# Optimization experiments

Measured on AMD Instinct MI355X. Metric: run time of the kernel, lower is better.

## Reference

```python
import jax, jax.numpy as jnp
import numpy as np

N = 100_000   # nodes (batched over G graphs)
E = 3_200_000 # edges (avg degree 32)
G = 64        # graphs in the batch
IN_FEATS, H1, H3, NUM_CLASSES = 64, 64, 64, 2


def setup_inputs() -> dict:
    key = jax.random.key(0)
    ks = jax.random.split(key, 11)
    return {
        "in_feat": jax.random.normal(ks[0], (N, IN_FEATS), jnp.float32),
        "edge_weights": jax.random.uniform(ks[1], (E,), jnp.float32, 1e-3, 1.0),
        "W1": jax.random.normal(ks[2], (IN_FEATS, H1), jnp.float32) / np.sqrt(IN_FEATS),
        "b1": jnp.zeros((H1,), jnp.float32),
        "W2": jax.random.normal(ks[3], (H1, H3), jnp.float32) / np.sqrt(H1),
        "b2": jnp.zeros((H3,), jnp.float32),
        "Wc": jax.random.normal(ks[4], (H3, NUM_CLASSES), jnp.float32) / np.sqrt(H3),
        "bc": jnp.zeros((NUM_CLASSES,), jnp.float32),
        "edge_src": jax.random.randint(ks[5], (E,), 0, N, jnp.int32),
        "edge_dst": jax.random.randint(ks[6], (E,), 0, N, jnp.int32),
        "graph_ids": jnp.sort(jax.random.randint(ks[7], (N,), 0, G, jnp.int32)),
    }


def reference(in_feat, edge_weights, W1, b1, W2, b2, Wc, bc,
              edge_src, edge_dst, graph_ids):
    # EdgeWeightNorm(norm='right'): w_e / (sum of weights into dst(e))
    deg_w = jax.ops.segment_sum(edge_weights, edge_dst, num_segments=N)  # [N]
    nw = edge_weights / deg_w[edge_dst]                                  # [E]

    # unweighted in-degree used by SAGEConv 'gcn' aggregator
    deg = jax.ops.segment_sum(jnp.ones((E,), jnp.float32), edge_dst, num_segments=N)  # [N]

    def sage_gcn(h, W, b):
        # weighted neighbor sum: sum_e nw_e * h[src_e] scattered to dst
        msg = h[edge_src] * nw[:, None]                                  # [E, F]
        neigh = jax.ops.segment_sum(msg, edge_dst, num_segments=N)      # [N, F]
        h_neigh = (neigh + h) / (deg[:, None] + 1.0)                     # gcn: include self, /(deg+1)
        return h_neigh @ W + b                                           # fc_neigh + bias

    h = jax.nn.relu(sage_gcn(in_feat, W1, b1))
    h = jax.nn.relu(sage_gcn(h, W2, b2))

    # dgl.mean_nodes: per-graph mean of node features
    counts = jax.ops.segment_sum(jnp.ones((N,), jnp.float32), graph_ids, num_segments=G)
    hg = jax.ops.segment_sum(h, graph_ids, num_segments=G) / jnp.maximum(counts, 1.0)[:, None]

    return hg @ Wc + bc  # [G, num_classes]
```

## Files before the change

### kernel.cpp

```cpp
#include <hip/hip_runtime.h>
#include <hip/hip_fp16.h>


#define CH2  4096
#define BK   1024
#define NB   128
#define CAPB 5120
#define CAPP 6144
#define SRCMASK ((1 << 18) - 1)
#define SRC17   0x1FFFFu

__device__ __forceinline__ float readlane_f(float v, int l) {
    return __int_as_float(__builtin_amdgcn_readlane(__float_as_int(v), l));
}

__device__ __forceinline__ int2 ntload_i2(const int2* p) {
    unsigned long long r = __builtin_nontemporal_load((const unsigned long long*)p);
    return make_int2((int)(unsigned)(r & 0xffffffffull), (int)(unsigned)(r >> 32));
}

__device__ __forceinline__ void ntstore_f2(float2* p, float2 v) {
    union { float2 f; unsigned long long u; } c;
    c.f = v;
    __builtin_nontemporal_store(c.u, (unsigned long long*)p);
}

__global__ void k_cvt(const float4* __restrict__ x, uint2* __restrict__ xh, int n4) {
    int i = blockIdx.x * blockDim.x + threadIdx.x;
    if (i >= n4) return;
    float4 v = x[i];
    __half2 a = __floats2half2_rn(v.x, v.y);
    __half2 b = __floats2half2_rn(v.z, v.w);
    uint2 r;
    r.x = *(const unsigned*)&a;
    r.y = *(const unsigned*)&b;
    xh[i] = r;
}

__global__ __launch_bounds__(512) void k_binfill2(
        const int* __restrict__ esrc, const int* __restrict__ edst,
        const float* __restrict__ ew, int* __restrict__ cursor,
        int2* __restrict__ bsw, int E, int B) {
    __shared__ int2 stg[CH2];
    __shared__ int h[BK];
    __shared__ int lcur[BK];
    __shared__ int gb[BK];
    __shared__ int sc[512];
    const int tid = threadIdx.x;

    for (int i = tid; i < BK; i += 512) h[i] = 0;
    __syncthreads();
    int e0 = blockIdx.x * CH2;
    int e1 = min(E, e0 + CH2);
    for (int e = e0 + tid; e < e1; e += 512)
        atomicAdd(&h[edst[e] >> 7], 1);
    __syncthreads();
    int a0 = h[2 * tid], a1 = h[2 * tid + 1];
    int s  = a0 + a1;
    sc[tid] = s;
    __syncthreads();
    for (int off = 1; off < 512; off <<= 1) {
        int t = (tid >= off) ? sc[tid - off] : 0;
        __syncthreads();
        sc[tid] += t;
        __syncthreads();
    }
    int base = sc[tid] - s;
    lcur[2 * tid]     = base;
    lcur[2 * tid + 1] = base + a0;
    gb[2 * tid]     = a0 ? atomicAdd(&cursor[2 * tid],     a0) : 0;
    gb[2 * tid + 1] = a1 ? atomicAdd(&cursor[2 * tid + 1], a1) : 0;
    __syncthreads();
    for (int e = e0 + tid; e < e1; e += 512) {
        int d = edst[e];
        int b = d >> 7;
        int p = atomicAdd(&lcur[b], 1);
        stg[p] = make_int2(((d & 127) << 18) | esrc[e], __float_as_int(ew[e]));
    }
    __syncthreads();
    const int wid = tid >> 6, lane = tid & 63;
    for (int b = wid; b < B; b += 8) {
        int len = h[b];
        if (!len) continue;
        int lb = lcur[b] - len;
        int g  = gb[b];
        int wlen = min(len, CAPB - g);
        if (wlen <= 0) continue;
        size_t gbase = (size_t)b * CAPB + g;
        for (int i = lane; i < wlen; i += 64)
            bsw[gbase + i] = stg[lb + i];
    }
}

__global__ __launch_bounds__(512) void k_csrsort(
        const int2* __restrict__ bsw, const int* __restrict__ cursor,
        unsigned* __restrict__ csr, int* __restrict__ off, int* __restrict__ fill,
        int N) {
    __shared__ unsigned se[CAPP];
    __shared__ int cur[NB];
    __shared__ int pfx[NB];
    __shared__ int tot;
    const int b = blockIdx.x, tid = threadIdx.x;
    for (int i = tid; i < CAPP; i += 512) se[i] = 0u;
    if (tid < NB) cur[tid] = 0;
    __syncthreads();
    const int cnt = min(cursor[b], CAPB);
    const int2* __restrict__ eb = bsw + (size_t)b * CAPB;
    for (int i = tid; i < cnt; i += 512)
        atomicAdd(&cur[eb[i].x >> 18], 1);
    __syncthreads();
    int pc = 0;
    if (tid < NB) {
        int c0 = cur[tid & ~1], c1 = cur[tid | 1];
        pc = (max(c0, c1) + 7) & ~7;
        pfx[tid] = pc;
    }
    __syncthreads();
    for (int o = 1; o < NB; o <<= 1) {
        int t = 0;
        if (tid < NB && tid >= o) t = pfx[tid - o];
        __syncthreads();
        if (tid < NB) pfx[tid] += t;
        __syncthreads();
    }
    if (tid < NB) {
        int excl = pfx[tid] - pc;
        int node = b * NB + tid;
        if (node < N) { off[node] = b * CAPP + excl; fill[node] = cur[tid]; }
        cur[tid] = excl;
        if (tid == NB - 1) tot = min(pfx[tid], CAPP);
    }
    __syncthreads();
    for (int i = tid; i < cnt; i += 512) {
        int2 e = eb[i];
        int p = atomicAdd(&cur[e.x >> 18], 1);
        unsigned h15 = (unsigned)__half_as_ushort(
                           __float2half_rn(__int_as_float(e.y))) & 0x7FFFu;
        if (p < CAPP)
            se[p] = ((unsigned)e.x & SRC17) | (h15 << 17);
    }
    __syncthreads();
    const int T = tot;
    unsigned* __restrict__ cb = csr + (size_t)b * CAPP;
    for (int i = tid; i < T; i += 512) cb[i] = se[i];
}

__global__ void k_fill_pad(const int* __restrict__ esrc, const int* __restrict__ edst,
                           const float* __restrict__ ew, int* __restrict__ fill,
                           int2* __restrict__ csr, int E, int CAP) {
    int e = blockIdx.x * blockDim.x + threadIdx.x;
    if (e < E) {
        int d = edst[e];
        int p = atomicAdd(&fill[d], 1);
        if (p < CAP)
            csr[(size_t)d * CAP + p] = make_int2(esrc[e], __float_as_int(ew[e]));
    }
}

__global__ void k_cnt(const int* __restrict__ edst, int* __restrict__ cnt, int E) {
    int e = blockIdx.x * blockDim.x + threadIdx.x;
    if (e < E) atomicAdd(&cnt[edst[e]], 1);
}

__global__ void k_off(const int* __restrict__ cnt, int* __restrict__ off,
                      int* __restrict__ fill, int* __restrict__ cursor, int N) {
    int i    = blockIdx.x * blockDim.x + threadIdx.x;
    int lane = threadIdx.x & 63;
    int c    = (i < N) ? cnt[i] : 0;
    int pref = c;
    #pragma unroll
    for (int d = 1; d < 64; d <<= 1) {
        int t = __shfl_up(pref, d);
        if (lane >= d) pref += t;
    }
    int total = __shfl(pref, 63);
    int base  = 0;
    if (lane == 63) base = atomicAdd(cursor, total);
    base = __shfl(base, 63);
    if (i < N) {
        int p = base + pref - c;
        off[i]  = p;
        fill[i] = p;
    }
}

__global__ void k_fill(const int* __restrict__ esrc, const int* __restrict__ edst,
                       const float* __restrict__ ew, int* __restrict__ fill,
                       int2* __restrict__ csr, int E) {
    int e = blockIdx.x * blockDim.x + threadIdx.x;
    if (e < E) {
        int d = edst[e];
        int p = atomicAdd(&fill[d], 1);
        csr[p] = make_int2(esrc[e], __float_as_int(ew[e]));
    }
}

__global__ __launch_bounds__(256, 6) void k_agg_p(
        const unsigned* __restrict__ xh, const int* __restrict__ off,
        const int* __restrict__ cnt_arr, const unsigned* __restrict__ csr,
        float* __restrict__ agg, int N) {
    const int lane = threadIdx.x & 63;
    const int slot = lane >> 5;
    const int f8   = lane & 31;
    const int wq   = (blockIdx.x * blockDim.x + threadIdx.x) >> 6;
    const int nw   = (gridDim.x * blockDim.x) >> 6;
    const int npair = (N + 1) >> 1;

    for (int pr = wq; pr < npair; pr += nw) {
        const int  node  = 2 * pr + slot;
        const bool valid = node < N;
        const int  cnt_s = valid ? cnt_arr[node] : 0;
        const int  st_s  = valid ? off[node] : 0;
        const int  cA = __builtin_amdgcn_readlane(cnt_s, 0);
        const int  cB = __builtin_amdgcn_readlane(cnt_s, 32);
        const int  pc = (max(cA, cB) + 7) & ~7;

        float2 acc = {0.f, 0.f};
        float  sw  = 0.f;
        const unsigned* __restrict__ pS = csr + st_s;
        for (int k = 0; k < pc; k += 8) {
            uint4 e0 = *(const uint4*)(pS + k);
            uint4 e1 = *(const uint4*)(pS + k + 4);
            unsigned ev[8] = {e0.x, e0.y, e0.z, e0.w, e1.x, e1.y, e1.z, e1.w};
            float    w[8];
            unsigned u[8];
            #pragma unroll
            for (int t = 0; t < 8; ++t) {
                unsigned e = ev[t];
                w[t] = __half2float(__ushort_as_half((unsigned short)(e >> 17)));
                u[t] = xh[((e & SRC17) << 5) | (unsigned)f8];
            }
            #pragma unroll
            for (int t = 0; t < 8; ++t) {
                float2 v = __half22float2(*(const __half2*)&u[t]);
                acc.x = fmaf(w[t], v.x, acc.x);
                acc.y = fmaf(w[t], v.y, acc.y);
                sw += w[t];
            }
        }
        if (valid) {
            float invw = (sw > 0.f) ? (1.f / sw) : 0.f;
            float invd = 1.f / ((float)cnt_s + 1.f);
            unsigned us = xh[((unsigned)node << 5) | (unsigned)f8];
            float2 xs = __half22float2(*(const __half2*)&us);
            float2 hn;
            hn.x = (acc.x * invw + xs.x) * invd;
            hn.y = (acc.y * invw + xs.y) * invd;
            ntstore_f2(&((float2*)agg)[(size_t)node * 32 + f8], hn);
        }
    }
}

__global__ __launch_bounds__(256, 4) void k_agg_f(
        const unsigned* __restrict__ xh, const int* __restrict__ off,
        const int* __restrict__ cnt_arr, const int2* __restrict__ csr,
        float* __restrict__ agg, int N, int CAP) {
    const int lane   = threadIdx.x & 63;
    const int slot   = lane >> 5;
    const int f8     = lane & 31;
    const int wave   = (blockIdx.x * blockDim.x + threadIdx.x) >> 6;
    const int nwaves = (gridDim.x * blockDim.x) >> 6;

    int node  = wave;
    int cnt_p = 0, start_p = 0;
    if (node < N) {
        cnt_p   = cnt_arr[node];
        start_p = (CAP > 0) ? node * CAP : off[node];
        if (CAP > 0) cnt_p = min(cnt_p, CAP);
    }
    for (; node < N; node += nwaves) {
        const int cnt = cnt_p, start = start_p;
        int nn = node + nwaves;
        if (nn < N) {
            cnt_p   = cnt_arr[nn];
            start_p = (CAP > 0) ? nn * CAP : off[nn];
            if (CAP > 0) cnt_p = min(cnt_p, CAP);
        }
        int2 ee = make_int2(0, 0);
        if (lane < cnt) ee = ntload_i2(&csr[start + lane]);
        float2 acc0 = {0.f, 0.f}, acc1 = {0.f, 0.f};
        float  sw = 0.0f;
        for (int bk = 0; bk < cnt; bk += 64) {
            int   s_l = ee.x;
            float w_l = __int_as_float(ee.y);
            int2 en = make_int2(0, 0);
            int  rem = cnt - bk - 64;
            if (lane < rem) en = ntload_i2(&csr[start + bk + 64 + lane]);
            sw += w_l;
            #pragma unroll
            for (int half = 0; half < 2; ++half) {
                float    w[16];
                unsigned u[16];
                #pragma unroll
                for (int k = 0; k < 16; ++k) {
                    int idx = half * 32 + 2 * k + slot;
                    int s   = __shfl(s_l, idx);
                    w[k]    = __shfl(w_l, idx);
                    u[k]    = xh[(size_t)s * 32 + f8];
                }
                #pragma unroll
                for (int k = 0; k < 16; k += 2) {
                    float2 v0 = __half22float2(*(const __half2*)&u[k]);
                    float2 v1 = __half22float2(*(const __half2*)&u[k + 1]);
                    acc0.x = fmaf(w[k],     v0.x, acc0.x);
                    acc0.y = fmaf(w[k],     v0.y, acc0.y);
                    acc1.x = fmaf(w[k + 1], v1.x, acc1.x);
                    acc1.y = fmaf(w[k + 1], v1.y, acc1.y);
                }
            }
            ee = en;
        }
        acc0.x += acc1.x; acc0.y += acc1.y;
        acc0.x += __shfl_xor(acc0.x, 32);
        acc0.y += __shfl_xor(acc0.y, 32);
        #pragma unroll
        for (int mask = 1; mask <= 32; mask <<= 1) sw += __shfl_xor(sw, mask);
        float invw = (sw > 0.0f) ? (1.0f / sw) : 0.0f;
        float invd = 1.0f / ((float)cnt + 1.0f);
        if (lane < 32) {
            unsigned us = xh[(size_t)node * 32 + f8];
            float2 xs = __half22float2(*(const __half2*)&us);
            float2 hn;
            hn.x = (acc0.x * invw + xs.x) * invd;
            hn.y = (acc0.y * invw + xs.y) * invd;
            ntstore_f2(&((float2*)agg)[(size_t)node * 32 + f8], hn);
        }
    }
}

__global__ __launch_bounds__(256) void k_fc(
        const float* __restrict__ agg, const float* __restrict__ W,
        const float* __restrict__ b, __half* __restrict__ outh, int N) {
    const int lane   = threadIdx.x & 63;
    const int wave   = (blockIdx.x * blockDim.x + threadIdx.x) >> 6;
    const int nwaves = (gridDim.x * blockDim.x) >> 6;
    float wc[64];
    #pragma unroll
    for (int f = 0; f < 64; ++f) wc[f] = W[f * 64 + lane];
    const float bias = b[lane];
    for (int node = wave; node < N; node += nwaves) {
        float hn = agg[(size_t)node * 64 + lane];
        float o0 = bias, o1 = 0.f, o2 = 0.f, o3 = 0.f;
        #pragma unroll
        for (int f = 0; f < 64; f += 4) {
            o0 = fmaf(readlane_f(hn, f),     wc[f],     o0);
            o1 = fmaf(readlane_f(hn, f + 1), wc[f + 1], o1);
            o2 = fmaf(readlane_f(hn, f + 2), wc[f + 2], o2);
            o3 = fmaf(readlane_f(hn, f + 3), wc[f + 3], o3);
        }
        float o = fmaxf((o0 + o1) + (o2 + o3), 0.0f);
        outh[(size_t)node * 64 + lane] = __float2half_rn(o);
    }
}

__global__ __launch_bounds__(256) void k_fcpool(
        const float* __restrict__ agg, const float* __restrict__ W,
        const float* __restrict__ b, const int* __restrict__ gid,
        float* __restrict__ hg, float* __restrict__ cntg, int N) {
    const int lane   = threadIdx.x & 63;
    const int wave   = (blockIdx.x * blockDim.x + threadIdx.x) >> 6;
    const int nwaves = (gridDim.x * blockDim.x) >> 6;
    float wc[64];
    #pragma unroll
    for (int f = 0; f < 64; ++f) wc[f] = W[f * 64 + lane];
    const float bias = b[lane];
    const int per   = (N + nwaves - 1) / nwaves;
    const int start = wave * per;
    const int end   = min(N, start + per);
    if (start >= N) return;

    int   curg = -1;
    float acc  = 0.0f;
    int   c    = 0;
    for (int node = start; node < end; ++node) {
        float hn = agg[(size_t)node * 64 + lane];
        float o0 = bias, o1 = 0.f, o2 = 0.f, o3 = 0.f;
        #pragma unroll
        for (int f = 0; f < 64; f += 4) {
            o0 = fmaf(readlane_f(hn, f),     wc[f],     o0);
            o1 = fmaf(readlane_f(hn, f + 1), wc[f + 1], o1);
            o2 = fmaf(readlane_f(hn, f + 2), wc[f + 2], o2);
            o3 = fmaf(readlane_f(hn, f + 3), wc[f + 3], o3);
        }
        float o = fmaxf((o0 + o1) + (o2 + o3), 0.0f);
        int g = gid[node];
        if (g != curg) {
            if (c > 0) {
                atomicAdd(&hg[curg * 64 + lane], acc);
                if (lane == 0) atomicAdd(&cntg[curg], (float)c);
            }
            curg = g; acc = 0.0f; c = 0;
        }
        acc += o;
        ++c;
    }
    if (c > 0) {
        atomicAdd(&hg[curg * 64 + lane], acc);
        if (lane == 0) atomicAdd(&cntg[curg], (float)c);
    }
}

__global__ void k_out(const float* __restrict__ hg, const float* __restrict__ cntg,
                      const float* __restrict__ Wc, const float* __restrict__ bc,
                      float* __restrict__ out, int G) {
    int t = blockIdx.x * blockDim.x + threadIdx.x;
    if (t >= G * 2) return;
    int g = t >> 1, c = t & 1;
    float ct = fmaxf(cntg[g], 1.0f);
    float o  = bc[c];
    for (int f = 0; f < 64; ++f)
        o += (hg[g * 64 + f] / ct) * Wc[f * 2 + c];
    out[t] = o;
}

extern "C" void kernel_launch(void* const* d_in, const int* in_sizes, int n_in,
                              void* d_out, int out_size, void* d_ws, size_t ws_size,
                              hipStream_t stream) {
    const float* in_feat = (const float*)d_in[0];
    const float* ew      = (const float*)d_in[1];
    const float* W1      = (const float*)d_in[2];
    const float* b1      = (const float*)d_in[3];
    const float* W2      = (const float*)d_in[4];
    const float* b2      = (const float*)d_in[5];
    const float* Wc      = (const float*)d_in[6];
    const float* bc      = (const float*)d_in[7];
    const int*   esrc    = (const int*)d_in[8];
    const int*   edst    = (const int*)d_in[9];
    const int*   gid     = (const int*)d_in[10];

    const int E = in_sizes[1];
    const int N = in_sizes[10];
    const int G = out_size / 2;
    float* outp = (float*)d_out;

    auto alignup = [](size_t x) { return (x + 15) & ~(size_t)15; };
    char* base = (char*)d_ws;
    const int FC_BLK = 1024, AGG_BLK = 2048;
    const int n4 = N * 16;

    const int B     = (N + NB - 1) / NB;
    const int NBLK2 = (E + CH2 - 1) / CH2;

    size_t zhdr  = ((size_t)G * 64 + G + BK) * 4;
    size_t o_off = alignup(zhdr);
    size_t o_fil = o_off + alignup((size_t)N * 4);
    size_t o_bsw = o_fil + alignup((size_t)N * 4);
    size_t o_csr = o_bsw + alignup((size_t)B * CAPB * 8);
    size_t o_t1  = o_csr + alignup((size_t)B * CAPP * 4);
    size_t o_t2  = o_t1 + alignup((size_t)N * 64 * 4);
    size_t o_xh  = o_t2 + alignup((size_t)N * 64 * 4);
    size_t o_th  = o_xh + alignup((size_t)N * 64 * 2);
    size_t needB = o_th + (size_t)N * 64 * 2;

    bool cap_ok = ((size_t)E / B) + 512 < CAPB && N <= (1 << 17);

    if (ws_size >= needB && B <= BK && cap_ok) {
        float*    hg     = (float*)base;
        float*    cntg   = hg + (size_t)G * 64;
        int*      cursor = (int*)(cntg + G);
        int*      off    = (int*)(base + o_off);
        int*      fill   = (int*)(base + o_fil);
        int2*     bsw    = (int2*)(base + o_bsw);
        unsigned* csr    = (unsigned*)(base + o_csr);
        float*    t1     = (float*)(base + o_t1);
        float*    t2     = (float*)(base + o_t2);
        unsigned* xh0    = (unsigned*)(base + o_xh);
        __half*   th1    = (__half*)(base + o_th);

        hipMemsetAsync(d_ws, 0, zhdr, stream);
        k_cvt     <<<(n4 + 255) / 256, 256, 0, stream>>>((const float4*)in_feat, (uint2*)xh0, n4);
        k_binfill2<<<NBLK2, 512, 0, stream>>>(esrc, edst, ew, cursor, bsw, E, B);
        k_csrsort <<<B, 512, 0, stream>>>(bsw, cursor, csr, off, fill, N);
        k_agg_p <<<AGG_BLK, 256, 0, stream>>>(xh0, off, fill, csr, t1, N);
        k_fc    <<<FC_BLK, 256, 0, stream>>>(t1, W1, b1, th1, N);
        k_agg_p <<<AGG_BLK, 256, 0, stream>>>((const unsigned*)th1, off, fill, csr, t2, N);
        k_fcpool<<<FC_BLK, 256, 0, stream>>>(t2, W2, b2, gid, hg, cntg, N);
        k_out   <<<1, 128, 0, stream>>>(hg, cntg, Wc, bc, outp, G);
        return;
    }

    const int CAP = 96;
    size_t hdr    = ((size_t)G * 64 + G + 1 + N) * 4;
    size_t needB2 = alignup(hdr) + alignup((size_t)N * CAP * 8)
                  + alignup((size_t)N * 64 * 4) * 2
                  + alignup((size_t)N * 64 * 2) * 2;
    if (ws_size >= needB2) {
        size_t o = 0;
        float* hg     = (float*)(base + o);
        float* cntg   = hg + (size_t)G * 64;
        int*   fill   = (int*)(cntg + G) + 1;
        o += alignup(hdr);
        int2*     csr = (int2*)(base + o);    o += alignup((size_t)N * CAP * 8);
        float*    t1  = (float*)(base + o);   o += alignup((size_t)N * 64 * 4);
        float*    t2  = (float*)(base + o);   o += alignup((size_t)N * 64 * 4);
        unsigned* xh0 = (unsigned*)(base + o); o += alignup((size_t)N * 64 * 2);
        __half*   th1 = (__half*)(base + o);

        hipMemsetAsync(d_ws, 0, hdr, stream);
        k_cvt     <<<(n4 + 255) / 256, 256, 0, stream>>>((const float4*)in_feat, (uint2*)xh0, n4);
        k_fill_pad<<<(E + 255) / 256, 256, 0, stream>>>(esrc, edst, ew, fill, csr, E, CAP);
        k_agg_f <<<AGG_BLK, 256, 0, stream>>>(xh0, (const int*)nullptr, fill, csr, t1, N, CAP);
        k_fc    <<<FC_BLK, 256, 0, stream>>>(t1, W1, b1, th1, N);
        k_agg_f <<<AGG_BLK, 256, 0, stream>>>((const unsigned*)th1, (const int*)nullptr, fill, csr, t2, N, CAP);
        k_fcpool<<<FC_BLK, 256, 0, stream>>>(t2, W2, b2, gid, hg, cntg, N);
        k_out   <<<1, 128, 0, stream>>>(hg, cntg, Wc, bc, outp, G);
        return;
    }

    {
        size_t o = 0;
        float* hg     = (float*)(base + o);
        float* cntg   = hg + (size_t)G * 64;
        int*   cursor = (int*)(cntg + G);
        int*   cnt    = cursor + 1;
        o += alignup(hdr);
        int*      off  = (int*)(base + o);    o += alignup((size_t)N * 4);
        int*      fill = (int*)(base + o);    o += alignup((size_t)N * 4);
        int2*     csr  = (int2*)(base + o);   o += alignup((size_t)E * 8);
        float*    t1   = (float*)(base + o);  o += alignup((size_t)N * 64 * 4);
        float*    t2   = (float*)(base + o);  o += alignup((size_t)N * 64 * 4);
        unsigned* xh0  = (unsigned*)(base + o); o += alignup((size_t)N * 64 * 2);
        __half*   th1  = (__half*)(base + o);

        hipMemsetAsync(d_ws, 0, hdr, stream);
        k_cvt <<<(n4 + 255) / 256, 256, 0, stream>>>((const float4*)in_feat, (uint2*)xh0, n4);
        k_cnt <<<(E + 255) / 256, 256, 0, stream>>>(edst, cnt, E);
        k_off <<<(N + 255) / 256, 256, 0, stream>>>(cnt, off, fill, cursor, N);
        k_fill<<<(E + 255) / 256, 256, 0, stream>>>(esrc, edst, ew, fill, csr, E);
        k_agg_f <<<AGG_BLK, 256, 0, stream>>>(xh0, off, cnt, csr, t1, N, 0);
        k_fc    <<<FC_BLK, 256, 0, stream>>>(t1, W1, b1, th1, N);
        k_agg_f <<<AGG_BLK, 256, 0, stream>>>((const unsigned*)th1, off, cnt, csr, t2, N, 0);
        k_fcpool<<<FC_BLK, 256, 0, stream>>>(t2, W2, b2, gid, hg, cntg, N);
        k_out   <<<1, 128, 0, stream>>>(hg, cntg, Wc, bc, outp, G);
    }
}
```

Measured before the change: 402.3 us.

## Replace two-pass bucketed CSR sort with count/scan/atomic-scatter CSR build

```diff
diff --git a/kernel.cpp b/kernel.cpp
--- a/kernel.cpp
+++ b/kernel.cpp
@@ -2,13 +2,7 @@
 #include <hip/hip_fp16.h>
 
 
-#define CH2  4096
-#define BK   1024
-#define NB   128
-#define CAPB 5120
-#define CAPP 6144
-#define SRCMASK ((1 << 18) - 1)
-#define SRC17   0x1FFFFu
+#define SRC17 0x1FFFFu
 
 __device__ __forceinline__ float readlane_f(float v, int l) {
     return __int_as_float(__builtin_amdgcn_readlane(__float_as_int(v), l));
@@ -37,112 +31,50 @@
     xh[i] = r;
 }
 
-__global__ __launch_bounds__(512) void k_binfill2(
-        const int* __restrict__ esrc, const int* __restrict__ edst,
-        const float* __restrict__ ew, int* __restrict__ cursor,
-        int2* __restrict__ bsw, int E, int B) {
-    __shared__ int2 stg[CH2];
-    __shared__ int h[BK];
-    __shared__ int lcur[BK];
-    __shared__ int gb[BK];
-    __shared__ int sc[512];
-    const int tid = threadIdx.x;
-
-    for (int i = tid; i < BK; i += 512) h[i] = 0;
-    __syncthreads();
-    int e0 = blockIdx.x * CH2;
-    int e1 = min(E, e0 + CH2);
-    for (int e = e0 + tid; e < e1; e += 512)
-        atomicAdd(&h[edst[e] >> 7], 1);
-    __syncthreads();
-    int a0 = h[2 * tid], a1 = h[2 * tid + 1];
-    int s  = a0 + a1;
-    sc[tid] = s;
-    __syncthreads();
-    for (int off = 1; off < 512; off <<= 1) {
-        int t = (tid >= off) ? sc[tid - off] : 0;
-        __syncthreads();
-        sc[tid] += t;
-        __syncthreads();
-    }
-    int base = sc[tid] - s;
-    lcur[2 * tid]     = base;
-    lcur[2 * tid + 1] = base + a0;
-    gb[2 * tid]     = a0 ? atomicAdd(&cursor[2 * tid],     a0) : 0;
-    gb[2 * tid + 1] = a1 ? atomicAdd(&cursor[2 * tid + 1], a1) : 0;
-    __syncthreads();
-    for (int e = e0 + tid; e < e1; e += 512) {
-        int d = edst[e];
-        int b = d >> 7;
-        int p = atomicAdd(&lcur[b], 1);
-        stg[p] = make_int2(((d & 127) << 18) | esrc[e], __float_as_int(ew[e]));
-    }
-    __syncthreads();
-    const int wid = tid >> 6, lane = tid & 63;
-    for (int b = wid; b < B; b += 8) {
-        int len = h[b];
-        if (!len) continue;
-        int lb = lcur[b] - len;
-        int g  = gb[b];
-        int wlen = min(len, CAPB - g);
-        if (wlen <= 0) continue;
-        size_t gbase = (size_t)b * CAPB + g;
-        for (int i = lane; i < wlen; i += 64)
-            bsw[gbase + i] = stg[lb + i];
-    }
-}
-
-__global__ __launch_bounds__(512) void k_csrsort(
-        const int2* __restrict__ bsw, const int* __restrict__ cursor,
-        unsigned* __restrict__ csr, int* __restrict__ off, int* __restrict__ fill,
-        int N) {
-    __shared__ unsigned se[CAPP];
-    __shared__ int cur[NB];
-    __shared__ int pfx[NB];
-    __shared__ int tot;
-    const int b = blockIdx.x, tid = threadIdx.x;
-    for (int i = tid; i < CAPP; i += 512) se[i] = 0u;
-    if (tid < NB) cur[tid] = 0;
-    __syncthreads();
-    const int cnt = min(cursor[b], CAPB);
-    const int2* __restrict__ eb = bsw + (size_t)b * CAPB;
-    for (int i = tid; i < cnt; i += 512)
-        atomicAdd(&cur[eb[i].x >> 18], 1);
-    __syncthreads();
-    int pc = 0;
-    if (tid < NB) {
-        int c0 = cur[tid & ~1], c1 = cur[tid | 1];
+__global__ void k_cnt(const int* __restrict__ edst, int* __restrict__ cnt, int E) {
+    int e = blockIdx.x * blockDim.x + threadIdx.x;
+    if (e < E) atomicAdd(&cnt[edst[e]], 1);
+}
+
+__global__ __launch_bounds__(256) void k_offp(
+        const int* __restrict__ cnt, int* __restrict__ off,
+        int* __restrict__ cursor, int N) {
+    const int i     = blockIdx.x * blockDim.x + threadIdx.x;
+    const int npair = (N + 1) >> 1;
+    const int lane  = threadIdx.x & 63;
+    int sz = 0, pc = 0;
+    if (i < npair) {
+        int c0 = cnt[2 * i];
+        int c1 = (2 * i + 1 < N) ? cnt[2 * i + 1] : 0;
         pc = (max(c0, c1) + 7) & ~7;
-        pfx[tid] = pc;
-    }
-    __syncthreads();
-    for (int o = 1; o < NB; o <<= 1) {
-        int t = 0;
-        if (tid < NB && tid >= o) t = pfx[tid - o];
-        __syncthreads();
-        if (tid < NB) pfx[tid] += t;
-        __syncthreads();
-    }
-    if (tid < NB) {
-        int excl = pfx[tid] - pc;
-        int node = b * NB + tid;
-        if (node < N) { off[node] = b * CAPP + excl; fill[node] = cur[tid]; }
-        cur[tid] = excl;
-        if (tid == NB - 1) tot = min(pfx[tid], CAPP);
-    }
-    __syncthreads();
-    for (int i = tid; i < cnt; i += 512) {
-        int2 e = eb[i];
-        int p = atomicAdd(&cur[e.x >> 18], 1);
-        unsigned h15 = (unsigned)__half_as_ushort(
-                           __float2half_rn(__int_as_float(e.y))) & 0x7FFFu;
-        if (p < CAPP)
-            se[p] = ((unsigned)e.x & SRC17) | (h15 << 17);
-    }
-    __syncthreads();
-    const int T = tot;
-    unsigned* __restrict__ cb = csr + (size_t)b * CAPP;
-    for (int i = tid; i < T; i += 512) cb[i] = se[i];
+        sz = 2 * pc;
+    }
+    int pref = sz;
+    #pragma unroll
+    for (int d = 1; d < 64; d <<= 1) {
+        int t = __shfl_up(pref, d);
+        if (lane >= d) pref += t;
+    }
+    int total = __shfl(pref, 63);
+    int base  = 0;
+    if (lane == 63 && total > 0) base = atomicAdd(cursor, total);
+    base = __shfl(base, 63);
+    if (i < npair) {
+        int b = base + pref - sz;
+        off[2 * i] = b;
+        if (2 * i + 1 < N) off[2 * i + 1] = b + pc;
+    }
+}
+
+__global__ void k_fillp(const int* __restrict__ esrc, const int* __restrict__ edst,
+                        const float* __restrict__ ew, const int* __restrict__ off,
+                        int* __restrict__ fill, unsigned* __restrict__ csr, int E) {
+    int e = blockIdx.x * blockDim.x + threadIdx.x;
+    if (e >= E) return;
+    int d = edst[e];
+    int p = atomicAdd(&fill[d], 1);
+    unsigned h15 = (unsigned)__half_as_ushort(__float2half_rn(ew[e])) & 0x7FFFu;
+    csr[off[d] + p] = ((unsigned)esrc[e] & SRC17) | (h15 << 17);
 }
 
 __global__ void k_fill_pad(const int* __restrict__ esrc, const int* __restrict__ edst,
@@ -155,11 +87,6 @@
         if (p < CAP)
             csr[(size_t)d * CAP + p] = make_int2(esrc[e], __float_as_int(ew[e]));
     }
-}
-
-__global__ void k_cnt(const int* __restrict__ edst, int* __restrict__ cnt, int E) {
-    int e = blockIdx.x * blockDim.x + threadIdx.x;
-    if (e < E) atomicAdd(&cnt[edst[e]], 1);
 }
 
 __global__ void k_off(const int* __restrict__ cnt, int* __restrict__ off,
@@ -437,30 +364,26 @@
     char* base = (char*)d_ws;
     const int FC_BLK = 1024, AGG_BLK = 2048;
     const int n4 = N * 16;
-
-    const int B     = (N + NB - 1) / NB;
-    const int NBLK2 = (E + CH2 - 1) / CH2;
-
-    size_t zhdr  = ((size_t)G * 64 + G + BK) * 4;
+    const int npair = (N + 1) >> 1;
+
+    size_t csr_cap = 2 * (size_t)E + 8 * (size_t)N;
+
+    size_t zhdr  = ((size_t)G * 64 + G + 4 + 2 * (size_t)N) * 4;
     size_t o_off = alignup(zhdr);
-    size_t o_fil = o_off + alignup((size_t)N * 4);
-    size_t o_bsw = o_fil + alignup((size_t)N * 4);
-    size_t o_csr = o_bsw + alignup((size_t)B * CAPB * 8);
-    size_t o_t1  = o_csr + alignup((size_t)B * CAPP * 4);
+    size_t o_csr = o_off + alignup((size_t)N * 4);
+    size_t o_t1  = o_csr + alignup(csr_cap * 4);
     size_t o_t2  = o_t1 + alignup((size_t)N * 64 * 4);
     size_t o_xh  = o_t2 + alignup((size_t)N * 64 * 4);
     size_t o_th  = o_xh + alignup((size_t)N * 64 * 2);
     size_t needB = o_th + (size_t)N * 64 * 2;
 
-    bool cap_ok = ((size_t)E / B) + 512 < CAPB && N <= (1 << 17);
-
-    if (ws_size >= needB && B <= BK && cap_ok) {
+    if (ws_size >= needB && N <= (1 << 17)) {
         float*    hg     = (float*)base;
         float*    cntg   = hg + (size_t)G * 64;
         int*      cursor = (int*)(cntg + G);
+        int*      cnt    = cursor + 4;
+        int*      fill   = cnt + N;
         int*      off    = (int*)(base + o_off);
-        int*      fill   = (int*)(base + o_fil);
-        int2*     bsw    = (int2*)(base + o_bsw);
         unsigned* csr    = (unsigned*)(base + o_csr);
         float*    t1     = (float*)(base + o_t1);
         float*    t2     = (float*)(base + o_t2);
@@ -468,12 +391,14 @@
         __half*   th1    = (__half*)(base + o_th);
 
         hipMemsetAsync(d_ws, 0, zhdr, stream);
-        k_cvt     <<<(n4 + 255) / 256, 256, 0, stream>>>((const float4*)in_feat, (uint2*)xh0, n4);
-        k_binfill2<<<NBLK2, 512, 0, stream>>>(esrc, edst, ew, cursor, bsw, E, B);
-        k_csrsort <<<B, 512, 0, stream>>>(bsw, cursor, csr, off, fill, N);
-        k_agg_p <<<AGG_BLK, 256, 0, stream>>>(xh0, off, fill, csr, t1, N);
+        hipMemsetAsync(csr, 0, csr_cap * 4, stream);
+        k_cvt  <<<(n4 + 255) / 256, 256, 0, stream>>>((const float4*)in_feat, (uint2*)xh0, n4);
+        k_cnt  <<<(E + 255) / 256, 256, 0, stream>>>(edst, cnt, E);
+        k_offp <<<(npair + 255) / 256, 256, 0, stream>>>(cnt, off, cursor, N);
+        k_fillp<<<(E + 255) / 256, 256, 0, stream>>>(esrc, edst, ew, off, fill, csr, E);
+        k_agg_p <<<AGG_BLK, 256, 0, stream>>>(xh0, off, cnt, csr, t1, N);
         k_fc    <<<FC_BLK, 256, 0, stream>>>(t1, W1, b1, th1, N);
-        k_agg_p <<<AGG_BLK, 256, 0, stream>>>((const unsigned*)th1, off, fill, csr, t2, N);
+        k_agg_p <<<AGG_BLK, 256, 0, stream>>>((const unsigned*)th1, off, cnt, csr, t2, N);
         k_fcpool<<<FC_BLK, 256, 0, stream>>>(t2, W2, b2, gid, hg, cntg, N);
         k_out   <<<1, 128, 0, stream>>>(hg, cntg, Wc, bc, outp, G);
         return;
```

Result: slower. 674.2 us (+67.6%).
